# Performance work log

Hardware: AMD Instinct MI355X
Metric: run time of the kernel (lower is better)

## Reference

```python
import jax, jax.numpy as jnp
import numpy as np

SEQ_LEN = 512
EMB_DIM = 2 * SEQ_LEN  # 1024
HIDDEN = 512
NUM_CLASSES = 10
BATCH = 256
VOCAB = 3


def setup_inputs() -> dict:
    key = jax.random.key(0)
    ks = jax.random.split(key, 16)
    def kaiming(k, shape, gain):
        fan_in = shape[0]
        return jax.random.normal(k, shape, dtype=jnp.float32) * (gain / np.sqrt(fan_in))
    tanh_g, sig_g, lin_g = np.sqrt(5.0 / 3.0), 1.0, 1.0
    return {
        "x": jax.random.randint(ks[0], (BATCH, SEQ_LEN), 0, VOCAB),
        "emb": jax.random.normal(ks[1], (VOCAB, EMB_DIM), dtype=jnp.float32),
        "W_gx": kaiming(ks[2], (EMB_DIM, HIDDEN), tanh_g),
        "W_gh": kaiming(ks[3], (HIDDEN, HIDDEN), tanh_g),
        "b_g": jnp.zeros((HIDDEN,), jnp.float32),
        "W_ix": kaiming(ks[4], (EMB_DIM, HIDDEN), sig_g),
        "W_ih": kaiming(ks[5], (HIDDEN, HIDDEN), sig_g),
        "b_i": jnp.zeros((HIDDEN,), jnp.float32),
        "W_fx": kaiming(ks[6], (EMB_DIM, HIDDEN), sig_g),
        "W_fh": kaiming(ks[7], (HIDDEN, HIDDEN), sig_g),
        "b_f": jnp.zeros((HIDDEN,), jnp.float32),
        "W_ox": kaiming(ks[8], (EMB_DIM, HIDDEN), sig_g),
        "W_oh": kaiming(ks[9], (HIDDEN, HIDDEN), sig_g),
        "b_o": jnp.zeros((HIDDEN,), jnp.float32),
        "W_ph": kaiming(ks[10], (HIDDEN, NUM_CLASSES), lin_g),
        "b_p": jnp.zeros((NUM_CLASSES,), jnp.float32),
    }


def reference(x, emb, W_gx, W_gh, b_g, W_ix, W_ih, b_i,
              W_fx, W_fh, b_f, W_ox, W_oh, b_o, W_ph, b_p):
    # Embed all tokens: [B, T, E]
    xe = emb[x]
    B = xe.shape[0]
    # Precompute input projections for all gates once: [T, B, 4H]
    Wx = jnp.concatenate([W_gx, W_ix, W_fx, W_ox], axis=1)  # [E, 4H]
    Wh = jnp.concatenate([W_gh, W_ih, W_fh, W_oh], axis=1)  # [H, 4H]
    b = jnp.concatenate([b_g, b_i, b_f, b_o])               # [4H]
    xg = jnp.einsum('bte,ef->tbf', xe, Wx) + b               # [T, B, 4H]

    H = W_gh.shape[0]

    def step(carry, xg_t):
        h, c = carry
        gates = xg_t + h @ Wh  # [B, 4H]
        g = jnp.tanh(gates[:, 0*H:1*H])
        i = jax.nn.sigmoid(gates[:, 1*H:2*H])
        f = jax.nn.sigmoid(gates[:, 2*H:3*H])
        o = jax.nn.sigmoid(gates[:, 3*H:4*H])
        c = g * i + c * f
        h = jnp.tanh(c) * o
        return (h, c), None

    h0 = jnp.zeros((B, H), xe.dtype)
    c0 = jnp.zeros((B, H), xe.dtype)
    (h_t, _), _ = jax.lax.scan(step, (h0, c0), xg)
    p = h_t @ W_ph + b_p
    return jax.nn.log_softmax(p, axis=1)
```

## Files before the change

### kernel.cpp

```cpp
#include <hip/hip_runtime.h>


typedef __attribute__((ext_vector_type(8))) _Float16 f16x8;
typedef __attribute__((ext_vector_type(4))) float f32x4;
typedef __attribute__((ext_vector_type(4))) unsigned u32x4;

#define NTHR 256
constexpr int T_LEN = 512, EMB = 1024, HID = 512, NCLS = 10;
constexpr int GSIZE = 16;
constexpr int NGRP  = 16;
constexpr int BPG   = 16;
constexpr int UPC   = 32;
constexpr int COLS_PC = 128;
constexpr int GUNITS  = GSIZE * 128;
constexpr int GSTRIDE = 3 * GUNITS;

__device__ __forceinline__ float sigmf(float x)    { return 1.f / (1.f + __expf(-x)); }
__device__ __forceinline__ float tanhfast(float x) { return 1.f - 2.f / (__expf(2.f * x) + 1.f); }

__device__ __forceinline__ void ld_pair(const u32x4* p, u32x4& a, u32x4& b) {
  asm volatile("global_load_dwordx4 %0, %2, off sc0 sc1\n\t"
               "global_load_dwordx4 %1, %2, off offset:16 sc0 sc1"
               : "=&v"(a), "=&v"(b) : "v"(p) : "memory");
}
__device__ __forceinline__ void wait_vm0() {
  asm volatile("s_waitcnt vmcnt(0)" ::: "memory");
  __builtin_amdgcn_sched_barrier(0);
}
__device__ __forceinline__ void st16(u32x4* p, u32x4 v) {
  asm volatile("global_store_dwordx4 %0, %1, off sc0 sc1" :: "v"(p), "v"(v) : "memory");
}

__global__ __launch_bounds__(NTHR, 1) void lstm_fused(
    const int* __restrict__ xtok, const float* __restrict__ emb,
    const float* __restrict__ Wgx, const float* __restrict__ Wgh, const float* __restrict__ b_g,
    const float* __restrict__ Wix, const float* __restrict__ Wih, const float* __restrict__ b_i,
    const float* __restrict__ Wfx, const float* __restrict__ Wfh, const float* __restrict__ b_f,
    const float* __restrict__ Wox, const float* __restrict__ Woh, const float* __restrict__ b_o,
    const float* __restrict__ Wph, const float* __restrict__ b_p,
    float* __restrict__ out, u32x4* __restrict__ gb)
{
  const int tid  = threadIdx.x;
  const int wv   = tid >> 6;
  const int lane = tid & 63;
  const int q    = lane >> 4;
  const int c    = lane & 15;
  const int wg   = blockIdx.x;
  const int grp  = wg >> 4;
  const int cu   = wg & 15;

  __shared__ __align__(16) f32x4 pacc[2][4][8][64];
  __shared__ __align__(16) _Float16 hstw[4][128];
  __shared__ unsigned char xl[BPG][T_LEN];
  __shared__ float projl[3][COLS_PC];
  __shared__ float projp[3][COLS_PC];

  for (int idx = tid; idx < BPG * T_LEN; idx += NTHR) {
    int bl = idx >> 9, tt = idx & (T_LEN - 1);
    xl[bl][tt] = (unsigned char)xtok[(grp * BPG + bl) * T_LEN + tt];
  }

  {
    int cc = tid & 127, half = tid >> 7;
    int w2 = cc >> 5, nt = (cc >> 4) & 1, c2 = cc & 15;
    int gate = nt * 2 + (c2 >> 3);
    int j = cu * UPC + w2 * 8 + (c2 & 7);
    const float* Wx = gate == 0 ? Wgx : gate == 1 ? Wix : gate == 2 ? Wfx : Wox;
    const float* bb = gate == 0 ? b_g : gate == 1 ? b_i : gate == 2 ? b_f : b_o;
    int e0 = half * (EMB / 2);
    for (int v = 0; v < 3; ++v) {
      float s = half ? 0.f : bb[j];
      const float* er = emb + v * EMB + e0;
      const float* wp = Wx + e0 * HID + j;
      #pragma unroll 4
      for (int e = 0; e < EMB / 2; ++e) s = fmaf(er[e], wp[e * HID], s);
      (half ? projp : projl)[v][cc] = s;
    }
  }
  __syncthreads();
  for (int idx = tid; idx < 3 * COLS_PC; idx += NTHR) {
    int v = idx >> 7, cc = idx & 127;
    projl[v][cc] += projp[v][cc];
  }

  f16x8 Bf[8][4];
  {
    int g0 = c >> 3;
    #pragma unroll
    for (int n = 0; n < 8; ++n) {
      int gate = (n & 1) * 2 + g0;
      int j = cu * UPC + (n >> 1) * 8 + (c & 7);
      const float* W = gate == 0 ? Wgh : gate == 1 ? Wih : gate == 2 ? Wfh : Woh;
      #pragma unroll
      for (int kk = 0; kk < 4; ++kk) {
        f16x8 tmp;
        #pragma unroll
        for (int jj = 0; jj < 8; ++jj)
          tmp[jj] = (_Float16)W[((wv * 4 + kk) * 32 + q * 8 + jj) * HID + j];
        Bf[n][kk] = tmp;
      }
    }
  }

  float cst[4] = {0.f, 0.f, 0.f, 0.f};
  u32x4* ug = gb + grp * GSTRIDE;
  int br = 0;
  __syncthreads();

  for (int t = 0; t < T_LEN; ++t) {
    const int pl = t & 1;
    f32x4 accp[8] = {{0.f,0.f,0.f,0.f},{0.f,0.f,0.f,0.f},{0.f,0.f,0.f,0.f},{0.f,0.f,0.f,0.f},
                     {0.f,0.f,0.f,0.f},{0.f,0.f,0.f,0.f},{0.f,0.f,0.f,0.f},{0.f,0.f,0.f,0.f}};
    if (t > 0) {
      const unsigned tagv = (unsigned)t;
      const u32x4* rb = ug + br * GUNITS;
      u32x4 ua[4], ub[4];
      for (;;) {
        #pragma unroll
        for (int i = 0; i < 4; ++i)
          ld_pair(rb + (wv * 4 + i) * 128 + 2 * lane, ua[i], ub[i]);
        wait_vm0();
        bool ok = true;
        #pragma unroll
        for (int i = 0; i < 4; ++i)
          ok = ok && (ua[i][2] == tagv) && (ub[i][2] == tagv);
        if (__all((int)ok)) break;
        __builtin_amdgcn_s_sleep(1);
      }
      #pragma unroll
      for (int kk = 0; kk < 4; ++kk) {
        u32x4 av = {ua[kk][0], ua[kk][1], ub[kk][0], ub[kk][1]};
        f16x8 a;
        __builtin_memcpy(&a, &av, 16);
        #pragma unroll
        for (int n = 0; n < 8; ++n)
          accp[n] = __builtin_amdgcn_mfma_f32_16x16x32_f16(a, Bf[n][kk], accp[n], 0, 0, 0);
      }
    }
    #pragma unroll
    for (int n = 0; n < 8; ++n) pacc[pl][wv][n][lane] = accp[n];
    __syncthreads();
    f32x4 p00 = pacc[pl][0][wv * 2][lane],     p01 = pacc[pl][1][wv * 2][lane];
    f32x4 p02 = pacc[pl][2][wv * 2][lane],     p03 = pacc[pl][3][wv * 2][lane];
    f32x4 p10 = pacc[pl][0][wv * 2 + 1][lane], p11 = pacc[pl][1][wv * 2 + 1][lane];
    f32x4 p12 = pacc[pl][2][wv * 2 + 1][lane], p13 = pacc[pl][3][wv * 2 + 1][lane];
    f32x4 acc0 = (p00 + p01) + (p02 + p03);
    f32x4 acc1 = (p10 + p11) + (p12 + p13);

    bool lo8 = (c < 8);
    #pragma unroll
    for (int r = 0; r < 4; ++r) {
      int bl = q * 4 + r;
      int v = xl[bl][t];
      float p0 = acc0[r] + projl[v][wv * 32 + c];
      float p1 = acc1[r] + projl[v][wv * 32 + 16 + c];
      float p0x = __shfl_xor(p0, 8);
      float p1x = __shfl_xor(p1, 8);
      float gg = lo8 ? p0  : p0x;
      float ii = lo8 ? p0x : p0;
      float ff = lo8 ? p1  : p1x;
      float oo = lo8 ? p1x : p1;
      gg = tanhfast(gg); ii = sigmf(ii); ff = sigmf(ff); oo = sigmf(oo);
      float cn = fmaf(cst[r], ff, gg * ii);
      cst[r] = cn;
      float hv = tanhfast(cn) * oo;
      if (lo8) hstw[wv][bl * 8 + c] = (_Float16)hv;
    }

    int bw = (br + 1 == 3) ? 0 : br + 1;
    if (lane < 32) {
      const unsigned* hw = (const unsigned*)&hstw[wv][0];
      u32x4 pv = {hw[2 * lane], hw[2 * lane + 1], (unsigned)(t + 1), 0u};
      st16(ug + bw * GUNITS + cu * 128 + wv * 32 + lane, pv);
    }
    br = bw;
  }

  if (wv == 0) {
    const u32x4* rb = ug + 2 * GUNITS;
    int kt = lane >> 2, qa = lane & 3;
    const u32x4* p = rb + kt * 128 + 2 * (qa * 16 + cu);
    u32x4 a, b;
    for (;;) {
      ld_pair(p, a, b);
      wait_vm0();
      bool ok = (a[2] == (unsigned)T_LEN) && (b[2] == (unsigned)T_LEN);
      if (__all((int)ok)) break;
      __builtin_amdgcn_s_sleep(1);
    }
    _Float16 hh[8];
    unsigned hw2[4] = {a[0], a[1], b[0], b[1]};
    __builtin_memcpy(&hh[0], &hw2[0], 16);
    float pc[NCLS];
    #pragma unroll
    for (int k2 = 0; k2 < NCLS; ++k2) pc[k2] = 0.f;
    int jbase = kt * 32 + qa * 8;
    #pragma unroll
    for (int jj = 0; jj < 8; ++jj) {
      float hv = (float)hh[jj];
      const float* wr = Wph + (jbase + jj) * NCLS;
      #pragma unroll
      for (int k2 = 0; k2 < NCLS; ++k2) pc[k2] = fmaf(hv, wr[k2], pc[k2]);
    }
    #pragma unroll
    for (int off = 32; off > 0; off >>= 1) {
      #pragma unroll
      for (int k2 = 0; k2 < NCLS; ++k2) pc[k2] += __shfl_down(pc[k2], off);
    }
    if (lane == 0) {
      float mx = -1e30f;
      #pragma unroll
      for (int k2 = 0; k2 < NCLS; ++k2) { pc[k2] += b_p[k2]; mx = fmaxf(mx, pc[k2]); }
      float se = 0.f;
      #pragma unroll
      for (int k2 = 0; k2 < NCLS; ++k2) se += __expf(pc[k2] - mx);
      float ls = mx + __logf(se);
      int b2 = grp * BPG + cu;
      #pragma unroll
      for (int k2 = 0; k2 < NCLS; ++k2) out[b2 * NCLS + k2] = pc[k2] - ls;
    }
  }
}

extern "C" void kernel_launch(void* const* d_in, const int* in_sizes, int n_in,
                              void* d_out, int out_size, void* d_ws, size_t ws_size,
                              hipStream_t stream) {
  (void)in_sizes; (void)n_in; (void)out_size; (void)ws_size;
  const int*   x   = (const int*)d_in[0];
  const float* emb = (const float*)d_in[1];
  const float* Wgx = (const float*)d_in[2];
  const float* Wgh = (const float*)d_in[3];
  const float* bg  = (const float*)d_in[4];
  const float* Wix = (const float*)d_in[5];
  const float* Wih = (const float*)d_in[6];
  const float* bi  = (const float*)d_in[7];
  const float* Wfx = (const float*)d_in[8];
  const float* Wfh = (const float*)d_in[9];
  const float* bfv = (const float*)d_in[10];
  const float* Wox = (const float*)d_in[11];
  const float* Woh = (const float*)d_in[12];
  const float* bo  = (const float*)d_in[13];
  const float* Wph = (const float*)d_in[14];
  const float* bp  = (const float*)d_in[15];
  float* out = (float*)d_out;

  (void)hipMemsetAsync(d_ws, 0, (size_t)NGRP * GSTRIDE * 16, stream);
  lstm_fused<<<dim3(NGRP * GSIZE), dim3(NTHR), 0, stream>>>(
      x, emb, Wgx, Wgh, bg, Wix, Wih, bi, Wfx, Wfh, bfv,
      Wox, Woh, bo, Wph, bp, out, (u32x4*)d_ws);
}
```

Measured before the change: 1.801 ms.

## Process four batch groups per workgroup, interleaving their recurrent steps

Shrinks the grid from 256 to 64 workgroups, so each workgroup handles four batch groups (g0, g0+4, g0+8, g0+12) and reuses the same register-resident recurrent weights. Each time step loops over the four groups in turn, so the cross-workgroup flag polling for one group can overlap with compute on the others. In exchange, per-step work per workgroup grows about fourfold, serialised inside one CU. An extra barrier per group is added because the pacc shared buffer is no longer double-buffered. Only 64 CUs are used, which lowers parallelism.

```diff
diff --git a/kernel.cpp b/kernel.cpp
--- a/kernel.cpp
+++ b/kernel.cpp
@@ -12,6 +12,7 @@
 constexpr int BPG   = 16;
 constexpr int UPC   = 32;
 constexpr int COLS_PC = 128;
+constexpr int KG    = 4;
 constexpr int GUNITS  = GSIZE * 128;
 constexpr int GSTRIDE = 3 * GUNITS;
 
@@ -46,18 +47,22 @@
   const int q    = lane >> 4;
   const int c    = lane & 15;
   const int wg   = blockIdx.x;
-  const int grp  = wg >> 4;
+  const int g0   = wg >> 4;
   const int cu   = wg & 15;
 
-  __shared__ __align__(16) f32x4 pacc[2][4][8][64];
+  __shared__ __align__(16) f32x4 pacc[4][8][64];
   __shared__ __align__(16) _Float16 hstw[4][128];
-  __shared__ unsigned char xl[BPG][T_LEN];
+  __shared__ unsigned char xl[KG][BPG][T_LEN];
   __shared__ float projl[3][COLS_PC];
   __shared__ float projp[3][COLS_PC];
 
-  for (int idx = tid; idx < BPG * T_LEN; idx += NTHR) {
-    int bl = idx >> 9, tt = idx & (T_LEN - 1);
-    xl[bl][tt] = (unsigned char)xtok[(grp * BPG + bl) * T_LEN + tt];
+  #pragma unroll
+  for (int j = 0; j < KG; ++j) {
+    int g = g0 + 4 * j;
+    for (int idx = tid; idx < BPG * T_LEN; idx += NTHR) {
+      int bl = idx >> 9, tt = idx & (T_LEN - 1);
+      xl[j][bl][tt] = (unsigned char)xtok[(g * BPG + bl) * T_LEN + tt];
+    }
   }
 
   {
@@ -85,10 +90,10 @@
 
   f16x8 Bf[8][4];
   {
-    int g0 = c >> 3;
+    int gg0 = c >> 3;
     #pragma unroll
     for (int n = 0; n < 8; ++n) {
-      int gate = (n & 1) * 2 + g0;
+      int gate = (n & 1) * 2 + gg0;
       int j = cu * UPC + (n >> 1) * 8 + (c & 7);
       const float* W = gate == 0 ? Wgh : gate == 1 ? Wih : gate == 2 ? Wfh : Woh;
       #pragma unroll
@@ -102,122 +107,129 @@
     }
   }
 
-  float cst[4] = {0.f, 0.f, 0.f, 0.f};
-  u32x4* ug = gb + grp * GSTRIDE;
+  float cst[KG][4] = {};
   int br = 0;
   __syncthreads();
 
   for (int t = 0; t < T_LEN; ++t) {
-    const int pl = t & 1;
-    f32x4 accp[8] = {{0.f,0.f,0.f,0.f},{0.f,0.f,0.f,0.f},{0.f,0.f,0.f,0.f},{0.f,0.f,0.f,0.f},
-                     {0.f,0.f,0.f,0.f},{0.f,0.f,0.f,0.f},{0.f,0.f,0.f,0.f},{0.f,0.f,0.f,0.f}};
-    if (t > 0) {
-      const unsigned tagv = (unsigned)t;
-      const u32x4* rb = ug + br * GUNITS;
-      u32x4 ua[4], ub[4];
+    const int bw = (br + 1 == 3) ? 0 : br + 1;
+    #pragma unroll
+    for (int j = 0; j < KG; ++j) {
+      u32x4* ug = gb + (g0 + 4 * j) * GSTRIDE;
+      f32x4 accp[8] = {{0.f,0.f,0.f,0.f},{0.f,0.f,0.f,0.f},{0.f,0.f,0.f,0.f},{0.f,0.f,0.f,0.f},
+                       {0.f,0.f,0.f,0.f},{0.f,0.f,0.f,0.f},{0.f,0.f,0.f,0.f},{0.f,0.f,0.f,0.f}};
+      if (t > 0) {
+        const unsigned tagv = (unsigned)t;
+        const u32x4* rb = ug + br * GUNITS;
+        u32x4 ua[4], ub[4];
+        for (;;) {
+          #pragma unroll
+          for (int i = 0; i < 4; ++i)
+            ld_pair(rb + (wv * 4 + i) * 128 + 2 * lane, ua[i], ub[i]);
+          wait_vm0();
+          bool ok = true;
+          #pragma unroll
+          for (int i = 0; i < 4; ++i)
+            ok = ok && (ua[i][2] == tagv) && (ub[i][2] == tagv);
+          if (__all((int)ok)) break;
+          __builtin_amdgcn_s_sleep(1);
+        }
+        #pragma unroll
+        for (int kk = 0; kk < 4; ++kk) {
+          u32x4 av = {ua[kk][0], ua[kk][1], ub[kk][0], ub[kk][1]};
+          f16x8 a;
+          __builtin_memcpy(&a, &av, 16);
+          #pragma unroll
+          for (int n = 0; n < 8; ++n)
+            accp[n] = __builtin_amdgcn_mfma_f32_16x16x32_f16(a, Bf[n][kk], accp[n], 0, 0, 0);
+        }
+      }
+      __syncthreads();
+      #pragma unroll
+      for (int n = 0; n < 8; ++n) pacc[wv][n][lane] = accp[n];
+      __syncthreads();
+      f32x4 p00 = pacc[0][wv * 2][lane],     p01 = pacc[1][wv * 2][lane];
+      f32x4 p02 = pacc[2][wv * 2][lane],     p03 = pacc[3][wv * 2][lane];
+      f32x4 p10 = pacc[0][wv * 2 + 1][lane], p11 = pacc[1][wv * 2 + 1][lane];
+      f32x4 p12 = pacc[2][wv * 2 + 1][lane], p13 = pacc[3][wv * 2 + 1][lane];
+      f32x4 acc0 = (p00 + p01) + (p02 + p03);
+      f32x4 acc1 = (p10 + p11) + (p12 + p13);
+
+      bool lo8 = (c < 8);
+      #pragma unroll
+      for (int r = 0; r < 4; ++r) {
+        int bl = q * 4 + r;
+        int v = xl[j][bl][t];
+        float p0 = acc0[r] + projl[v][wv * 32 + c];
+        float p1 = acc1[r] + projl[v][wv * 32 + 16 + c];
+        float p0x = __shfl_xor(p0, 8);
+        float p1x = __shfl_xor(p1, 8);
+        float gg = lo8 ? p0  : p0x;
+        float ii = lo8 ? p0x : p0;
+        float ff = lo8 ? p1  : p1x;
+        float oo = lo8 ? p1x : p1;
+        gg = tanhfast(gg); ii = sigmf(ii); ff = sigmf(ff); oo = sigmf(oo);
+        float cn = fmaf(cst[j][r], ff, gg * ii);
+        cst[j][r] = cn;
+        float hv = tanhfast(cn) * oo;
+        if (lo8) hstw[wv][bl * 8 + c] = (_Float16)hv;
+      }
+
+      if (lane < 32) {
+        const unsigned* hw = (const unsigned*)&hstw[wv][0];
+        u32x4 pv = {hw[2 * lane], hw[2 * lane + 1], (unsigned)(t + 1), 0u};
+        st16(ug + bw * GUNITS + cu * 128 + wv * 32 + lane, pv);
+      }
+    }
+    br = bw;
+  }
+
+  if (wv == 0) {
+    #pragma unroll
+    for (int j = 0; j < KG; ++j) {
+      int g = g0 + 4 * j;
+      const u32x4* rb = gb + g * GSTRIDE + 2 * GUNITS;
+      int kt = lane >> 2, qa = lane & 3;
+      const u32x4* p = rb + kt * 128 + 2 * (qa * 16 + cu);
+      u32x4 a, b;
       for (;;) {
-        #pragma unroll
-        for (int i = 0; i < 4; ++i)
-          ld_pair(rb + (wv * 4 + i) * 128 + 2 * lane, ua[i], ub[i]);
+        ld_pair(p, a, b);
         wait_vm0();
-        bool ok = true;
-        #pragma unroll
-        for (int i = 0; i < 4; ++i)
-          ok = ok && (ua[i][2] == tagv) && (ub[i][2] == tagv);
+        bool ok = (a[2] == (unsigned)T_LEN) && (b[2] == (unsigned)T_LEN);
         if (__all((int)ok)) break;
         __builtin_amdgcn_s_sleep(1);
       }
-      #pragma unroll
-      for (int kk = 0; kk < 4; ++kk) {
-        u32x4 av = {ua[kk][0], ua[kk][1], ub[kk][0], ub[kk][1]};
-        f16x8 a;
-        __builtin_memcpy(&a, &av, 16);
-        #pragma unroll
-        for (int n = 0; n < 8; ++n)
-          accp[n] = __builtin_amdgcn_mfma_f32_16x16x32_f16(a, Bf[n][kk], accp[n], 0, 0, 0);
-      }
-    }
-    #pragma unroll
-    for (int n = 0; n < 8; ++n) pacc[pl][wv][n][lane] = accp[n];
-    __syncthreads();
-    f32x4 p00 = pacc[pl][0][wv * 2][lane],     p01 = pacc[pl][1][wv * 2][lane];
-    f32x4 p02 = pacc[pl][2][wv * 2][lane],     p03 = pacc[pl][3][wv * 2][lane];
-    f32x4 p10 = pacc[pl][0][wv * 2 + 1][lane], p11 = pacc[pl][1][wv * 2 + 1][lane];
-    f32x4 p12 = pacc[pl][2][wv * 2 + 1][lane], p13 = pacc[pl][3][wv * 2 + 1][lane];
-    f32x4 acc0 = (p00 + p01) + (p02 + p03);
-    f32x4 acc1 = (p10 + p11) + (p12 + p13);
-
-    bool lo8 = (c < 8);
-    #pragma unroll
-    for (int r = 0; r < 4; ++r) {
-      int bl = q * 4 + r;
-      int v = xl[bl][t];
-      float p0 = acc0[r] + projl[v][wv * 32 + c];
-      float p1 = acc1[r] + projl[v][wv * 32 + 16 + c];
-      float p0x = __shfl_xor(p0, 8);
-      float p1x = __shfl_xor(p1, 8);
-      float gg = lo8 ? p0  : p0x;
-      float ii = lo8 ? p0x : p0;
-      float ff = lo8 ? p1  : p1x;
-      float oo = lo8 ? p1x : p1;
-      gg = tanhfast(gg); ii = sigmf(ii); ff = sigmf(ff); oo = sigmf(oo);
-      float cn = fmaf(cst[r], ff, gg * ii);
-      cst[r] = cn;
-      float hv = tanhfast(cn) * oo;
-      if (lo8) hstw[wv][bl * 8 + c] = (_Float16)hv;
-    }
-
-    int bw = (br + 1 == 3) ? 0 : br + 1;
-    if (lane < 32) {
-      const unsigned* hw = (const unsigned*)&hstw[wv][0];
-      u32x4 pv = {hw[2 * lane], hw[2 * lane + 1], (unsigned)(t + 1), 0u};
-      st16(ug + bw * GUNITS + cu * 128 + wv * 32 + lane, pv);
-    }
-    br = bw;
-  }
-
-  if (wv == 0) {
-    const u32x4* rb = ug + 2 * GUNITS;
-    int kt = lane >> 2, qa = lane & 3;
-    const u32x4* p = rb + kt * 128 + 2 * (qa * 16 + cu);
-    u32x4 a, b;
-    for (;;) {
-      ld_pair(p, a, b);
-      wait_vm0();
-      bool ok = (a[2] == (unsigned)T_LEN) && (b[2] == (unsigned)T_LEN);
-      if (__all((int)ok)) break;
-      __builtin_amdgcn_s_sleep(1);
-    }
-    _Float16 hh[8];
-    unsigned hw2[4] = {a[0], a[1], b[0], b[1]};
-    __builtin_memcpy(&hh[0], &hw2[0], 16);
-    float pc[NCLS];
-    #pragma unroll
-    for (int k2 = 0; k2 < NCLS; ++k2) pc[k2] = 0.f;
-    int jbase = kt * 32 + qa * 8;
-    #pragma unroll
-    for (int jj = 0; jj < 8; ++jj) {
-      float hv = (float)hh[jj];
-      const float* wr = Wph + (jbase + jj) * NCLS;
-      #pragma unroll
-      for (int k2 = 0; k2 < NCLS; ++k2) pc[k2] = fmaf(hv, wr[k2], pc[k2]);
-    }
-    #pragma unroll
-    for (int off = 32; off > 0; off >>= 1) {
-      #pragma unroll
-      for (int k2 = 0; k2 < NCLS; ++k2) pc[k2] += __shfl_down(pc[k2], off);
-    }
-    if (lane == 0) {
-      float mx = -1e30f;
-      #pragma unroll
-      for (int k2 = 0; k2 < NCLS; ++k2) { pc[k2] += b_p[k2]; mx = fmaxf(mx, pc[k2]); }
-      float se = 0.f;
-      #pragma unroll
-      for (int k2 = 0; k2 < NCLS; ++k2) se += __expf(pc[k2] - mx);
-      float ls = mx + __logf(se);
-      int b2 = grp * BPG + cu;
-      #pragma unroll
-      for (int k2 = 0; k2 < NCLS; ++k2) out[b2 * NCLS + k2] = pc[k2] - ls;
+      _Float16 hh[8];
+      unsigned hw2[4] = {a[0], a[1], b[0], b[1]};
+      __builtin_memcpy(&hh[0], &hw2[0], 16);
+      float pc[NCLS];
+      #pragma unroll
+      for (int k2 = 0; k2 < NCLS; ++k2) pc[k2] = 0.f;
+      int jbase = kt * 32 + qa * 8;
+      #pragma unroll
+      for (int jj = 0; jj < 8; ++jj) {
+        float hv = (float)hh[jj];
+        const float* wr = Wph + (jbase + jj) * NCLS;
+        #pragma unroll
+        for (int k2 = 0; k2 < NCLS; ++k2) pc[k2] = fmaf(hv, wr[k2], pc[k2]);
+      }
+      #pragma unroll
+      for (int off = 32; off > 0; off >>= 1) {
+        #pragma unroll
+        for (int k2 = 0; k2 < NCLS; ++k2) pc[k2] += __shfl_down(pc[k2], off);
+      }
+      if (lane == 0) {
+        float mx = -1e30f;
+        #pragma unroll
+        for (int k2 = 0; k2 < NCLS; ++k2) { pc[k2] += b_p[k2]; mx = fmaxf(mx, pc[k2]); }
+        float se = 0.f;
+        #pragma unroll
+        for (int k2 = 0; k2 < NCLS; ++k2) se += __expf(pc[k2] - mx);
+        float ls = mx + __logf(se);
+        int b2 = g * BPG + cu;
+        #pragma unroll
+        for (int k2 = 0; k2 < NCLS; ++k2) out[b2 * NCLS + k2] = pc[k2] - ls;
+      }
     }
   }
 }
@@ -245,7 +257,7 @@
   float* out = (float*)d_out;
 
   (void)hipMemsetAsync(d_ws, 0, (size_t)NGRP * GSTRIDE * 16, stream);
-  lstm_fused<<<dim3(NGRP * GSIZE), dim3(NTHR), 0, stream>>>(
+  lstm_fused<<<dim3(NGRP * GSIZE / KG), dim3(NTHR), 0, stream>>>(
       x, emb, Wgx, Wgh, bg, Wix, Wih, bi, Wfx, Wfh, bfv,
       Wox, Woh, bo, Wph, bp, out, (u32x4*)d_ws);
 }
```

New measurement: 5.217 ms. +189.6%, slower.
